# Kernel optimization log

Hardware: AMD Instinct MI355X
Metric: run time of the kernel (lower is better)

## Reference

```python
import jax, jax.numpy as jnp
import numpy as np

DIM, HEADS, NB_FEATURES = 512, 8, 64
HEAD_DIM = DIM // HEADS


def setup_inputs() -> dict:
    key = jax.random.key(0)
    k_x, k_qkv, k_pm, k_wp, k_bp = jax.random.split(key, 5)
    B, N = 8, 4096
    x = jax.random.normal(k_x, (B, N, DIM), dtype=jnp.float32)
    # to_qkv: Linear(dim, 3*dim, bias=False) -> apply as x @ w_qkv
    w_qkv = jax.random.normal(k_qkv, (DIM, 3 * DIM), dtype=jnp.float32) * (1.0 / np.sqrt(DIM))
    # random projection buffer [H, D, F]
    proj_mat = jax.random.normal(k_pm, (HEADS, HEAD_DIM, NB_FEATURES), dtype=jnp.float32)
    # output projection Linear(dim, dim) with bias
    w_proj = jax.random.normal(k_wp, (DIM, DIM), dtype=jnp.float32) * (1.0 / np.sqrt(DIM))
    b_proj = jax.random.normal(k_bp, (DIM,), dtype=jnp.float32) * 0.01
    return {"x": x, "w_qkv": w_qkv, "proj_mat": proj_mat, "w_proj": w_proj, "b_proj": b_proj}


def _phi(t, proj_mat):
    # t: [B,N,H,D], proj_mat: [H,D,F] -> [B,N,H,F]
    return jax.nn.elu(jnp.einsum('bnhd,hdf->bnhf', t, proj_mat)) + 1.0


def reference(x, w_qkv, proj_mat, w_proj, b_proj):
    B, N, dim = x.shape
    H, D = HEADS, dim // HEADS
    qkv = x @ w_qkv  # [B,N,3*dim]
    q, k, v = jnp.split(qkv, 3, axis=-1)
    q = q.reshape(B, N, H, D)
    k = k.reshape(B, N, H, D)
    v = v.reshape(B, N, H, D)
    q_phi = _phi(q, proj_mat)  # [B,N,H,F]
    k_phi = _phi(k, proj_mat)  # [B,N,H,F]
    kv = jnp.einsum('bnhf,bnhd->bhfd', k_phi, v)  # [B,H,F,D]
    z = 1.0 / jnp.einsum('bnhf,bhf->bnh', q_phi, k_phi.sum(axis=1))  # [B,N,H]
    out = jnp.einsum('bnhf,bhfd,bnh->bnhd', q_phi, kv, z)  # [B,N,H,D]
    out = out.reshape(B, N, H * D)
    return out @ w_proj + b_proj
```

## Files before the change

kernel.cpp:

```cpp
#include <hip/hip_runtime.h>
#include <hip/hip_bf16.h>

typedef __bf16 bf16_t;
typedef __bf16 bf16x4 __attribute__((ext_vector_type(4)));
typedef __bf16 bf16x8 __attribute__((ext_vector_type(8)));
typedef float f32x2 __attribute__((ext_vector_type(2)));
typedef float f32x4 __attribute__((ext_vector_type(4)));

__device__ __forceinline__ void gload16(const void* g, void* l) {
  __builtin_amdgcn_global_load_lds((const __attribute__((address_space(1))) void*)g,
                                   (__attribute__((address_space(3))) void*)l, 16, 0, 0);
}

#define VMW(n) asm volatile("s_waitcnt vmcnt(" #n ")" ::: "memory")

__global__ __launch_bounds__(256) void prep_qk(const float* __restrict__ w_qkv,
                                               const float* __restrict__ proj,
                                               bf16_t* __restrict__ WeffT) {
  const int half = blockIdx.x >> 3, h = blockIdx.x & 7;
  const int i0 = blockIdx.y * 64;
  __shared__ float P[64 * 64];
  __shared__ float Wt[64][65];
  const int t = threadIdx.x;
  #pragma unroll
  for (int r = 0; r < 16; ++r) P[t + 256 * r] = proj[(size_t)h * 4096 + t + 256 * r];
  #pragma unroll
  for (int r = 0; r < 16; ++r) {
    const int idx = t + 256 * r;
    Wt[idx >> 6][idx & 63] =
        w_qkv[(size_t)(i0 + (idx >> 6)) * 1536 + half * 512 + h * 64 + (idx & 63)];
  }
  __syncthreads();
  const int i = t & 63, fg = t >> 6;
  for (int f = fg; f < 64; f += 4) {
    float s = 0.f;
    #pragma unroll
    for (int d = 0; d < 64; ++d) s += Wt[i][d] * P[d * 64 + f];
    WeffT[(size_t)(half * 512 + h * 64 + f) * 512 + i0 + i] = (bf16_t)s;
  }
}

__global__ __launch_bounds__(256) void prep_v(const float* __restrict__ w_qkv,
                                              bf16_t* __restrict__ WeffT) {
  __shared__ bf16_t tile[32][33];
  const int i0 = blockIdx.x * 32, n0 = blockIdx.y * 32;
  const int tn = threadIdx.x & 31, ti = threadIdx.x >> 5;
  #pragma unroll
  for (int p = 0; p < 4; ++p) {
    const int i = ti + p * 8;
    tile[i][tn] = (bf16_t)w_qkv[(size_t)(i0 + i) * 1536 + 1024 + n0 + tn];
  }
  __syncthreads();
  #pragma unroll
  for (int p = 0; p < 4; ++p) {
    const int n = ti + p * 8;
    WeffT[(size_t)(1024 + n0 + n) * 512 + i0 + tn] = tile[tn][n];
  }
}

__global__ __launch_bounds__(256) void cast_x(const f32x4* __restrict__ x,
                                              bf16x4* __restrict__ xb, int n4) {
  int i = blockIdx.x * 256 + threadIdx.x;
  if (i < n4) {
    f32x4 v = x[i];
    bf16x4 o;
    #pragma unroll
    for (int j = 0; j < 4; ++j) o[j] = (bf16_t)v[j];
    xb[i] = o;
  }
}

__global__ __launch_bounds__(256) void gemm_qkv(const bf16_t* __restrict__ x_bf,
                                                const bf16_t* __restrict__ WeffT,
                                                bf16_t* __restrict__ q_phi,
                                                bf16_t* __restrict__ kT,
                                                bf16_t* __restrict__ vT) {
  constexpr int K = 512, BK = 64;
  __shared__ alignas(16) char smem[65536];
  const int t = threadIdx.x, w = t >> 6, l = t & 63;
  const int hw = blockIdx.x;
  const int bid = (hw & 7) * 384 + (hw >> 3);
  const int tok_blk = bid / 12, cb = bid % 12;
  const size_t tok0 = (size_t)tok_blk * 128;
  const bool qpath = (cb < 4);
  const bf16_t* Pp = qpath ? (WeffT + (size_t)cb * 128 * 512) : (x_bf + tok0 * 512);
  const bf16_t* Qp = qpath ? (x_bf + tok0 * 512)
                           : (WeffT + (size_t)(512 + (cb - 4) * 128) * 512);

  const int wr = w >> 1, wc = w & 1;
  const int lrow = l & 15, lkb = l >> 4;
  const int st_r = l >> 3;
  const int st_c = ((l & 7) ^ st_r) * 8;
  size_t p_src[4], q_src[4];
  #pragma unroll
  for (int c = 0; c < 4; ++c) {
    const int q8 = c * 4 + w;
    p_src[c] = (size_t)(q8 * 8 + st_r) * K + st_c;
    q_src[c] = (size_t)(q8 * 8 + st_r) * K + st_c;
  }

  f32x4 acc[4][4];
  #pragma unroll
  for (int m = 0; m < 4; ++m)
    #pragma unroll
    for (int n = 0; n < 4; ++n) acc[m][n] = f32x4{0.f, 0.f, 0.f, 0.f};

  #pragma unroll
  for (int c = 0; c < 4; ++c) {
    const int q8 = c * 4 + w;
    gload16(Pp + p_src[c], smem + q8 * 1024);
    gload16(Qp + q_src[c], smem + 16384 + q8 * 1024);
  }
  __syncthreads();

  int cur = 0;
  for (int kt = 0; kt < K; kt += BK) {
    if (kt + BK < K) {
      char* nb = smem + (cur ^ 1) * 32768;
      #pragma unroll
      for (int c = 0; c < 4; ++c) {
        const int q8 = c * 4 + w;
        gload16(Pp + p_src[c] + kt + BK, nb + q8 * 1024);
        gload16(Qp + q_src[c] + kt + BK, nb + 16384 + q8 * 1024);
      }
    }
    const char* PsB = smem + cur * 32768;
    const char* QsB = PsB + 16384;
    bf16x8 pf[4][2], qf[4][2];
    #pragma unroll
    for (int m = 0; m < 4; ++m) {
      const int r = wr * 64 + m * 16 + lrow;
      #pragma unroll
      for (int kk = 0; kk < 2; ++kk) {
        const int kb = lkb + kk * 4;
        pf[m][kk] = *(const bf16x8*)(PsB + r * 128 + (((kb ^ (r & 7)) & 7) << 4));
      }
    }
    #pragma unroll
    for (int n = 0; n < 4; ++n) {
      const int r = wc * 64 + n * 16 + lrow;
      #pragma unroll
      for (int kk = 0; kk < 2; ++kk) {
        const int kb = lkb + kk * 4;
        qf[n][kk] = *(const bf16x8*)(QsB + r * 128 + (((kb ^ (r & 7)) & 7) << 4));
      }
    }
    #pragma unroll
    for (int m = 0; m < 4; ++m)
      #pragma unroll
      for (int n = 0; n < 4; ++n) {
        acc[m][n] = __builtin_amdgcn_mfma_f32_16x16x32_bf16(pf[m][0], qf[n][0], acc[m][n], 0, 0, 0);
        acc[m][n] = __builtin_amdgcn_mfma_f32_16x16x32_bf16(pf[m][1], qf[n][1], acc[m][n], 0, 0, 0);
      }
    __syncthreads();
    cur ^= 1;
  }

  bf16_t* ep = (bf16_t*)smem;
  const bool doElu = qpath || (cb < 8);
  #pragma unroll
  for (int n = 0; n < 4; ++n) {
    const int qc = wc * 64 + n * 16 + lrow;
    #pragma unroll
    for (int m = 0; m < 4; ++m) {
      const int pr0 = wr * 64 + m * 16 + lkb * 4;
      bf16x4 o;
      #pragma unroll
      for (int j = 0; j < 4; ++j) {
        float v = acc[m][n][j];
        if (doElu) v = v > 0.f ? v + 1.f : __expf(v);
        o[j] = (bf16_t)v;
      }
      const int u = pr0 >> 3;
      *(bf16x4*)((char*)ep + qc * 256 + ((u ^ (qc & 15)) << 4) + (pr0 & 7) * 2) = o;
    }
  }
  __syncthreads();
  #pragma unroll
  for (int i = 0; i < 8; ++i) {
    const int flat = i * 256 + t;
    const int qc2 = flat >> 4, u2 = flat & 15;
    bf16x8 vv = *(const bf16x8*)((char*)ep + qc2 * 256 + ((u2 ^ (qc2 & 15)) << 4));
    if (qpath) {
      *(bf16x8*)&q_phi[(tok0 + qc2) * 512 + cb * 128 + u2 * 8] = vv;
    } else {
      const int f512 = (cb - 4) * 128 + qc2;
      bf16_t* dst = (f512 < 512 ? kT + ((size_t)(tok0 >> 12) * 512 + f512) * 4096
                                : vT + ((size_t)(tok0 >> 12) * 512 + (f512 - 512)) * 4096) +
                    (tok0 & 4095) + u2 * 8;
      *(bf16x8*)dst = vv;
    }
  }
}

__global__ __launch_bounds__(256) void kv_mfma(const bf16_t* __restrict__ kT,
                                               const bf16_t* __restrict__ vT,
                                               float* __restrict__ kv,
                                               float* __restrict__ ksum) {
  const int bh = blockIdx.x;
  const int nbase = blockIdx.y * 512;
  __shared__ alignas(16) char smem[32768];
  const int t = threadIdx.x, w = t >> 6, l = t & 63;
  const int wr = w >> 1, wc = w & 1;
  const int lrow = l & 15, lkb = l >> 4;
  const int st_r = l >> 3;
  const int st_c = ((l & 7) ^ st_r) * 8;
  const bf16_t* Kp = kT + (size_t)bh * 64 * 4096;
  const bf16_t* Vp = vT + (size_t)bh * 64 * 4096;

  f32x4 acc[2][2];
  #pragma unroll
  for (int m = 0; m < 2; ++m)
    #pragma unroll
    for (int n = 0; n < 2; ++n) acc[m][n] = f32x4{0.f, 0.f, 0.f, 0.f};
  float ksf[2] = {0.f, 0.f};

  #pragma unroll
  for (int c = 0; c < 2; ++c) {
    const int q8 = w * 2 + c;
    gload16(Kp + (size_t)(q8 * 8 + st_r) * 4096 + nbase + st_c, smem + q8 * 1024);
    gload16(Vp + (size_t)(q8 * 8 + st_r) * 4096 + nbase + st_c, smem + 8192 + q8 * 1024);
  }
  __syncthreads();

  int cur = 0;
  for (int st = 0; st < 8; ++st) {
    if (st < 7) {
      char* nb = smem + (cur ^ 1) * 16384;
      const int nb2 = nbase + (st + 1) * 64;
      #pragma unroll
      for (int c = 0; c < 2; ++c) {
        const int q8 = w * 2 + c;
        gload16(Kp + (size_t)(q8 * 8 + st_r) * 4096 + nb2 + st_c, nb + q8 * 1024);
        gload16(Vp + (size_t)(q8 * 8 + st_r) * 4096 + nb2 + st_c, nb + 8192 + q8 * 1024);
      }
    }
    const char* KsB = smem + cur * 16384;
    const char* VsB = KsB + 8192;
    bf16x8 af[2][2], bf[2][2];
    #pragma unroll
    for (int m = 0; m < 2; ++m) {
      const int r = wr * 32 + m * 16 + lrow;
      #pragma unroll
      for (int kk = 0; kk < 2; ++kk) {
        const int kb = lkb + kk * 4;
        af[m][kk] = *(const bf16x8*)(KsB + r * 128 + (((kb ^ (r & 7)) & 7) << 4));
      }
    }
    #pragma unroll
    for (int n = 0; n < 2; ++n) {
      const int r = wc * 32 + n * 16 + lrow;
      #pragma unroll
      for (int kk = 0; kk < 2; ++kk) {
        const int kb = lkb + kk * 4;
        bf[n][kk] = *(const bf16x8*)(VsB + r * 128 + (((kb ^ (r & 7)) & 7) << 4));
      }
    }
    #pragma unroll
    for (int m = 0; m < 2; ++m)
      #pragma unroll
      for (int n = 0; n < 2; ++n) {
        acc[m][n] = __builtin_amdgcn_mfma_f32_16x16x32_bf16(af[m][0], bf[n][0], acc[m][n], 0, 0, 0);
        acc[m][n] = __builtin_amdgcn_mfma_f32_16x16x32_bf16(af[m][1], bf[n][1], acc[m][n], 0, 0, 0);
      }
    if (wc == 0) {
      #pragma unroll
      for (int m = 0; m < 2; ++m)
        #pragma unroll
        for (int kk = 0; kk < 2; ++kk)
          #pragma unroll
          for (int j = 0; j < 8; ++j) ksf[m] += (float)af[m][kk][j];
    }
    __syncthreads();
    cur ^= 1;
  }

  float* kvp = kv + (size_t)bh * 4096;
  #pragma unroll
  for (int m = 0; m < 2; ++m)
    #pragma unroll
    for (int n = 0; n < 2; ++n)
      #pragma unroll
      for (int j = 0; j < 4; ++j)
        atomicAdd(&kvp[(wr * 32 + m * 16 + lkb * 4 + j) * 64 + wc * 32 + n * 16 + lrow],
                  acc[m][n][j]);
  if (wc == 0) {
    #pragma unroll
    for (int m = 0; m < 2; ++m) {
      float s = ksf[m];
      s += __shfl_xor(s, 16);
      s += __shfl_xor(s, 32);
      if (l < 16) atomicAdd(&ksum[(size_t)bh * 64 + wr * 32 + m * 16 + l], s);
    }
  }
}

__global__ __launch_bounds__(256) void w2_kernel(const float* __restrict__ kv,
                                                 const float* __restrict__ w_proj,
                                                 bf16_t* __restrict__ W2T) {
  const int bh = blockIdx.x, b = bh >> 3, h = bh & 7;
  const int j0 = blockIdx.y * 64;
  const int t = threadIdx.x;
  __shared__ float kvs[64][64];
  __shared__ float wps[64][64];
  const float* kvp = kv + (size_t)bh * 4096;
  #pragma unroll
  for (int i = 0; i < 16; ++i) ((float*)kvs)[t + 256 * i] = kvp[t + 256 * i];
  {
    const int d = t >> 2, c16 = (t & 3) * 16;
    const float* src = w_proj + (size_t)(h * 64 + d) * 512 + j0 + c16;
    #pragma unroll
    for (int j = 0; j < 16; ++j) wps[d][c16 + j] = src[j];
  }
  __syncthreads();
  const int fq = t >> 4, jq = t & 15;
  float acc[4][4] = {};
  for (int d = 0; d < 64; ++d) {
    float kf[4], wj[4];
    #pragma unroll
    for (int i = 0; i < 4; ++i) kf[i] = kvs[fq * 4 + i][d];
    #pragma unroll
    for (int i = 0; i < 4; ++i) wj[i] = wps[d][jq * 4 + i];
    #pragma unroll
    for (int i = 0; i < 4; ++i)
      #pragma unroll
      for (int j = 0; j < 4; ++j) acc[i][j] += kf[i] * wj[j];
  }
  #pragma unroll
  for (int j = 0; j < 4; ++j)
    #pragma unroll
    for (int i = 0; i < 4; ++i)
      W2T[((size_t)b * 512 + j0 + jq * 4 + j) * 512 + h * 64 + fq * 4 + i] = (bf16_t)acc[i][j];
}

__global__ __launch_bounds__(256) void gemm_out(const bf16_t* __restrict__ W2T,
                                                const bf16_t* __restrict__ q_phi,
                                                const float* __restrict__ ksum,
                                                float* __restrict__ Cout,
                                                const float* __restrict__ bias) {
  __shared__ alignas(16) char smem[67584];
  const int t = threadIdx.x, w = t >> 6, l = t & 63;
  const int hw = blockIdx.x;
  const int bid = (hw & 7) * 128 + (hw >> 3);
  const int z = bid >> 7;
  const int rem = bid & 127;
  const int qblk = rem >> 2, pblk = rem & 3;
  const size_t tok0 = (size_t)qblk * 128;
  const int pj0 = pblk * 128;
  const bf16_t* Pp = W2T + ((size_t)z * 512 + pj0) * 512;

  const int wr = w >> 1, wc = w & 1;
  const int lrow = l & 15, lkb = l >> 4;
  const int st_r = l >> 3;
  const int st_c = ((l & 7) ^ st_r) * 8;
  const int token = t >> 1, half = t & 1;
  float* ks_lds = (float*)(smem + 65536);

  bf16x8 breg[4];
  auto loadB = [&](int c) {
    const bf16_t* p = q_phi + ((size_t)z * 4096 + tok0 + token) * 512 + c * 64 + half * 32;
    breg[0] = *(const bf16x8*)p;
    breg[1] = *(const bf16x8*)(p + 8);
    breg[2] = *(const bf16x8*)(p + 16);
    breg[3] = *(const bf16x8*)(p + 24);
  };
  auto stageA = [&](int s) {
    #pragma unroll
    for (int c = 0; c < 4; ++c) {
      const int q8 = c * 4 + w;
      gload16(Pp + (size_t)(q8 * 8 + st_r) * 512 + s * 64 + st_c,
              smem + (s & 1) * 16384 + q8 * 1024);
    }
  };
  auto procB = [&](int c) {
    const f32x4* ksv = (const f32x4*)(ks_lds + c * 64 + half * 32);
    float vals[32];
    float dot = 0.f;
    #pragma unroll
    for (int g = 0; g < 8; ++g) {
      const f32x4 kk = ksv[g];
      #pragma unroll
      for (int j = 0; j < 4; ++j) {
        const float v = (float)breg[g >> 1][(g & 1) * 4 + j];
        vals[g * 4 + j] = v;
        dot += v * kk[j];
      }
    }
    dot += __shfl_xor(dot, 1);
    const float zz = 1.f / dot;
    char* dst = smem + 32768 + (c & 1) * 16384;
    #pragma unroll
    for (int g = 0; g < 4; ++g) {
      bf16x8 o;
      #pragma unroll
      for (int j = 0; j < 8; ++j) o[j] = (bf16_t)(vals[g * 8 + j] * zz);
      const int uk = half * 4 + g;
      *(bf16x8*)(dst + token * 128 + ((uk ^ (token & 7)) << 4)) = o;
    }
  };

  {
    const f32x2 kk = *(const f32x2*)&ksum[(size_t)z * 512 + t * 2];
    *(f32x2*)&ks_lds[t * 2] = kk;
  }
  __syncthreads();
  loadB(0);
  stageA(0);
  procB(0);
  VMW(0);
  __syncthreads();

  f32x4 acc[4][4];
  #pragma unroll
  for (int m = 0; m < 4; ++m)
    #pragma unroll
    for (int n = 0; n < 4; ++n) acc[m][n] = f32x4{0.f, 0.f, 0.f, 0.f};

  for (int kt = 0; kt < 8; ++kt) {
    const char* PsB = smem + (kt & 1) * 16384;
    const char* QsB = smem + 32768 + (kt & 1) * 16384;
    bf16x8 pf[4][2], qf[4][2];
    #pragma unroll
    for (int m = 0; m < 4; ++m) {
      const int r = wr * 64 + m * 16 + lrow;
      #pragma unroll
      for (int kk = 0; kk < 2; ++kk) {
        const int kb = lkb + kk * 4;
        pf[m][kk] = *(const bf16x8*)(PsB + r * 128 + (((kb ^ (r & 7)) & 7) << 4));
      }
    }
    #pragma unroll
    for (int n = 0; n < 4; ++n) {
      const int r = wc * 64 + n * 16 + lrow;
      #pragma unroll
      for (int kk = 0; kk < 2; ++kk) {
        const int kb = lkb + kk * 4;
        qf[n][kk] = *(const bf16x8*)(QsB + r * 128 + (((kb ^ (r & 7)) & 7) << 4));
      }
    }
    if (kt + 1 < 8) { loadB(kt + 1); stageA(kt + 1); }
    #pragma unroll
    for (int m = 0; m < 4; ++m)
      #pragma unroll
      for (int n = 0; n < 4; ++n) {
        acc[m][n] = __builtin_amdgcn_mfma_f32_16x16x32_bf16(pf[m][0], qf[n][0], acc[m][n], 0, 0, 0);
        acc[m][n] = __builtin_amdgcn_mfma_f32_16x16x32_bf16(pf[m][1], qf[n][1], acc[m][n], 0, 0, 0);
      }
    if (kt + 1 < 8) { procB(kt + 1); VMW(0); }
    __syncthreads();
  }

  float* ep = (float*)smem;
  #pragma unroll
  for (int p = 0; p < 2; ++p) {
    if (p) __syncthreads();
    #pragma unroll
    for (int nn2 = 0; nn2 < 2; ++nn2) {
      const int n = p * 2 + nn2;
      const int r6 = wc * 32 + (n & 1) * 16 + lrow;
      #pragma unroll
      for (int m = 0; m < 4; ++m) {
        const int pr0 = wr * 64 + m * 16 + lkb * 4;
        f32x4 v = acc[m][n];
        const f32x4 bv = *(const f32x4*)&bias[pj0 + pr0];
        #pragma unroll
        for (int j = 0; j < 4; ++j) v[j] += bv[j];
        const int u = pr0 >> 2;
        *(f32x4*)((char*)ep + r6 * 512 + ((u ^ (r6 & 31)) << 4)) = v;
      }
    }
    __syncthreads();
    #pragma unroll
    for (int i = 0; i < 8; ++i) {
      const int flat = i * 256 + t;
      const int r6 = flat >> 5, u2 = flat & 31;
      f32x4 v = *(const f32x4*)((char*)ep + r6 * 512 + ((u2 ^ (r6 & 31)) << 4));
      const int qc = (r6 >> 5) * 64 + p * 32 + (r6 & 31);
      *(f32x4*)&Cout[((size_t)z * 4096 + tok0 + qc) * 512 + pj0 + u2 * 4] = v;
    }
  }
}

extern "C" void kernel_launch(void* const* d_in, const int* in_sizes, int n_in,
                              void* d_out, int out_size, void* d_ws, size_t ws_size,
                              hipStream_t stream) {
  const float* x      = (const float*)d_in[0];
  const float* w_qkv  = (const float*)d_in[1];
  const float* proj   = (const float*)d_in[2];
  const float* w_proj = (const float*)d_in[3];
  const float* b_proj = (const float*)d_in[4];
  float* out = (float*)d_out;
  char* ws = (char*)d_ws;

  bf16_t* x_bf  = (bf16_t*)(ws + 0);
  bf16_t* WeffT = (bf16_t*)(ws + 33554432);
  bf16_t* q_phi = (bf16_t*)(ws + 35127296);
  bf16_t* kT    = (bf16_t*)(ws + 68681728);
  bf16_t* vT    = (bf16_t*)(ws + 102236160);
  float*  kv    = (float*)(ws + 135790592);
  float*  ksum  = (float*)(ws + 136839168);
  bf16_t* W2T   = (bf16_t*)(ws + 136855552);

  prep_qk<<<dim3(16, 8), 256, 0, stream>>>(w_qkv, proj, WeffT);
  prep_v<<<dim3(16, 16), 256, 0, stream>>>(w_qkv, WeffT);
  cast_x<<<16384, 256, 0, stream>>>((const f32x4*)x, (bf16x4*)x_bf, 4194304);
  gemm_qkv<<<3072, 256, 0, stream>>>(x_bf, WeffT, q_phi, kT, vT);
  hipMemsetAsync(kv, 0, 1048576 + 16384, stream);
  kv_mfma<<<dim3(64, 8), 256, 0, stream>>>(kT, vT, kv, ksum);
  w2_kernel<<<dim3(64, 8), 256, 0, stream>>>(kv, w_proj, W2T);
  gemm_out<<<1024, 256, 0, stream>>>(W2T, q_phi, ksum, out, b_proj);
}
```

Measured before the change: 175.2 us.

## Fuse fp32-to-bf16 cast of x into QKV GEMM tile loading

Removes the standalone cast_x kernel and has gemm_qkv stage fp32 x tiles directly into shared memory, converting to bf16 when building MFMA fragments. The K tile shrinks to 32 with new swizzles for the fp32 and bf16 buffers. This saves a full pass that wrote and re-read a bf16 copy of x, but doubles the bytes of x pulled per GEMM tile and adds conversion work and more loop iterations and barriers.

```diff
diff --git a/kernel.cpp b/kernel.cpp
--- a/kernel.cpp
+++ b/kernel.cpp
@@ -58,46 +58,41 @@
   }
 }
 
-__global__ __launch_bounds__(256) void cast_x(const f32x4* __restrict__ x,
-                                              bf16x4* __restrict__ xb, int n4) {
-  int i = blockIdx.x * 256 + threadIdx.x;
-  if (i < n4) {
-    f32x4 v = x[i];
-    bf16x4 o;
-    #pragma unroll
-    for (int j = 0; j < 4; ++j) o[j] = (bf16_t)v[j];
-    xb[i] = o;
-  }
-}
-
-__global__ __launch_bounds__(256) void gemm_qkv(const bf16_t* __restrict__ x_bf,
+__global__ __launch_bounds__(256) void gemm_qkv(const float* __restrict__ x,
                                                 const bf16_t* __restrict__ WeffT,
                                                 bf16_t* __restrict__ q_phi,
                                                 bf16_t* __restrict__ kT,
                                                 bf16_t* __restrict__ vT) {
-  constexpr int K = 512, BK = 64;
-  __shared__ alignas(16) char smem[65536];
+  __shared__ alignas(16) char smem[49152];
   const int t = threadIdx.x, w = t >> 6, l = t & 63;
   const int hw = blockIdx.x;
   const int bid = (hw & 7) * 384 + (hw >> 3);
   const int tok_blk = bid / 12, cb = bid % 12;
   const size_t tok0 = (size_t)tok_blk * 128;
   const bool qpath = (cb < 4);
-  const bf16_t* Pp = qpath ? (WeffT + (size_t)cb * 128 * 512) : (x_bf + tok0 * 512);
-  const bf16_t* Qp = qpath ? (x_bf + tok0 * 512)
-                           : (WeffT + (size_t)(512 + (cb - 4) * 128) * 512);
+  const float* Xp = x + tok0 * 512;
+  const bf16_t* Wp = WeffT + (size_t)(qpath ? cb * 128 : 512 + (cb - 4) * 128) * 512;
 
   const int wr = w >> 1, wc = w & 1;
   const int lrow = l & 15, lkb = l >> 4;
-  const int st_r = l >> 3;
-  const int st_c = ((l & 7) ^ st_r) * 8;
-  size_t p_src[4], q_src[4];
-  #pragma unroll
-  for (int c = 0; c < 4; ++c) {
-    const int q8 = c * 4 + w;
-    p_src[c] = (size_t)(q8 * 8 + st_r) * K + st_c;
-    q_src[c] = (size_t)(q8 * 8 + st_r) * K + st_c;
-  }
+
+  const int sr8 = t >> 3, su8 = t & 7;
+  const int sr4 = t >> 2, su4 = t & 3;
+  const size_t fcol = (size_t)((su8 ^ (sr8 & 7)) * 4);
+  const size_t hcol = (size_t)((su4 ^ ((t >> 3) & 3)) * 8);
+
+  auto stageF = [&](int s) {
+    char* dst = smem + (s & 1) * 16384;
+    #pragma unroll
+    for (int c = 0; c < 4; ++c)
+      gload16(Xp + (size_t)(c * 32 + sr8) * 512 + s * 32 + fcol, dst + c * 4096 + t * 16);
+  };
+  auto stageH = [&](int s) {
+    char* dst = smem + 32768 + (s & 1) * 8192;
+    #pragma unroll
+    for (int c = 0; c < 2; ++c)
+      gload16(Wp + (size_t)(c * 64 + sr4) * 512 + s * 32 + hcol, dst + c * 4096 + t * 16);
+  };
 
   f32x4 acc[4][4];
   #pragma unroll
@@ -105,55 +100,49 @@
     #pragma unroll
     for (int n = 0; n < 4; ++n) acc[m][n] = f32x4{0.f, 0.f, 0.f, 0.f};
 
-  #pragma unroll
-  for (int c = 0; c < 4; ++c) {
-    const int q8 = c * 4 + w;
-    gload16(Pp + p_src[c], smem + q8 * 1024);
-    gload16(Qp + q_src[c], smem + 16384 + q8 * 1024);
-  }
-  __syncthreads();
-
-  int cur = 0;
-  for (int kt = 0; kt < K; kt += BK) {
-    if (kt + BK < K) {
-      char* nb = smem + (cur ^ 1) * 32768;
-      #pragma unroll
-      for (int c = 0; c < 4; ++c) {
-        const int q8 = c * 4 + w;
-        gload16(Pp + p_src[c] + kt + BK, nb + q8 * 1024);
-        gload16(Qp + q_src[c] + kt + BK, nb + 16384 + q8 * 1024);
-      }
-    }
-    const char* PsB = smem + cur * 32768;
-    const char* QsB = PsB + 16384;
-    bf16x8 pf[4][2], qf[4][2];
-    #pragma unroll
-    for (int m = 0; m < 4; ++m) {
-      const int r = wr * 64 + m * 16 + lrow;
-      #pragma unroll
-      for (int kk = 0; kk < 2; ++kk) {
-        const int kb = lkb + kk * 4;
-        pf[m][kk] = *(const bf16x8*)(PsB + r * 128 + (((kb ^ (r & 7)) & 7) << 4));
-      }
-    }
-    #pragma unroll
-    for (int n = 0; n < 4; ++n) {
-      const int r = wc * 64 + n * 16 + lrow;
-      #pragma unroll
-      for (int kk = 0; kk < 2; ++kk) {
-        const int kb = lkb + kk * 4;
-        qf[n][kk] = *(const bf16x8*)(QsB + r * 128 + (((kb ^ (r & 7)) & 7) << 4));
+  stageF(0); stageH(0);
+  __syncthreads();
+
+  for (int kt = 0; kt < 16; ++kt) {
+    if (kt + 1 < 16) { stageF(kt + 1); stageH(kt + 1); }
+    const char* Fs = smem + (kt & 1) * 16384;
+    const char* Hs = smem + 32768 + (kt & 1) * 8192;
+    bf16x8 pf[4], qf[4];
+    if (qpath) {
+      #pragma unroll
+      for (int m = 0; m < 4; ++m) {
+        const int r = wr * 64 + m * 16 + lrow;
+        pf[m] = *(const bf16x8*)(Hs + r * 64 + ((lkb ^ ((r >> 1) & 3)) << 4));
+      }
+      #pragma unroll
+      for (int n = 0; n < 4; ++n) {
+        const int r = wc * 64 + n * 16 + lrow;
+        const f32x4 a = *(const f32x4*)(Fs + r * 128 + (((2 * lkb) ^ (r & 7)) << 4));
+        const f32x4 b = *(const f32x4*)(Fs + r * 128 + (((2 * lkb + 1) ^ (r & 7)) << 4));
+        #pragma unroll
+        for (int j = 0; j < 4; ++j) { qf[n][j] = (bf16_t)a[j]; qf[n][4 + j] = (bf16_t)b[j]; }
+      }
+    } else {
+      #pragma unroll
+      for (int m = 0; m < 4; ++m) {
+        const int r = wr * 64 + m * 16 + lrow;
+        const f32x4 a = *(const f32x4*)(Fs + r * 128 + (((2 * lkb) ^ (r & 7)) << 4));
+        const f32x4 b = *(const f32x4*)(Fs + r * 128 + (((2 * lkb + 1) ^ (r & 7)) << 4));
+        #pragma unroll
+        for (int j = 0; j < 4; ++j) { pf[m][j] = (bf16_t)a[j]; pf[m][4 + j] = (bf16_t)b[j]; }
+      }
+      #pragma unroll
+      for (int n = 0; n < 4; ++n) {
+        const int r = wc * 64 + n * 16 + lrow;
+        qf[n] = *(const bf16x8*)(Hs + r * 64 + ((lkb ^ ((r >> 1) & 3)) << 4));
       }
     }
     #pragma unroll
     for (int m = 0; m < 4; ++m)
       #pragma unroll
-      for (int n = 0; n < 4; ++n) {
-        acc[m][n] = __builtin_amdgcn_mfma_f32_16x16x32_bf16(pf[m][0], qf[n][0], acc[m][n], 0, 0, 0);
-        acc[m][n] = __builtin_amdgcn_mfma_f32_16x16x32_bf16(pf[m][1], qf[n][1], acc[m][n], 0, 0, 0);
-      }
+      for (int n = 0; n < 4; ++n)
+        acc[m][n] = __builtin_amdgcn_mfma_f32_16x16x32_bf16(pf[m], qf[n], acc[m][n], 0, 0, 0);
     __syncthreads();
-    cur ^= 1;
   }
 
   bf16_t* ep = (bf16_t*)smem;
@@ -492,19 +481,17 @@
   float* out = (float*)d_out;
   char* ws = (char*)d_ws;
 
-  bf16_t* x_bf  = (bf16_t*)(ws + 0);
-  bf16_t* WeffT = (bf16_t*)(ws + 33554432);
-  bf16_t* q_phi = (bf16_t*)(ws + 35127296);
-  bf16_t* kT    = (bf16_t*)(ws + 68681728);
-  bf16_t* vT    = (bf16_t*)(ws + 102236160);
-  float*  kv    = (float*)(ws + 135790592);
-  float*  ksum  = (float*)(ws + 136839168);
-  bf16_t* W2T   = (bf16_t*)(ws + 136855552);
+  bf16_t* WeffT = (bf16_t*)(ws + 0);
+  bf16_t* q_phi = (bf16_t*)(ws + 1572864);
+  bf16_t* kT    = (bf16_t*)(ws + 35127296);
+  bf16_t* vT    = (bf16_t*)(ws + 68681728);
+  float*  kv    = (float*)(ws + 102236160);
+  float*  ksum  = (float*)(ws + 103284736);
+  bf16_t* W2T   = (bf16_t*)(ws + 103301120);
 
   prep_qk<<<dim3(16, 8), 256, 0, stream>>>(w_qkv, proj, WeffT);
   prep_v<<<dim3(16, 16), 256, 0, stream>>>(w_qkv, WeffT);
-  cast_x<<<16384, 256, 0, stream>>>((const f32x4*)x, (bf16x4*)x_bf, 4194304);
-  gemm_qkv<<<3072, 256, 0, stream>>>(x_bf, WeffT, q_phi, kT, vT);
+  gemm_qkv<<<3072, 256, 0, stream>>>(x, WeffT, q_phi, kT, vT);
   hipMemsetAsync(kv, 0, 1048576 + 16384, stream);
   kv_mfma<<<dim3(64, 8), 256, 0, stream>>>(kT, vT, kv, ksum);
   w2_kernel<<<dim3(64, 8), 256, 0, stream>>>(kv, w_proj, W2T);
```

After: 169.9 us (median of 2 runs). 3.0% less time.
